# Kernel tuning notes

Measured on AMD Instinct MI355X. Metric: run time of the kernel, lower is better.

The kernel has to match this reference:

```python
import jax, jax.numpy as jnp
import numpy as np
import math

EMBED_DIM = 1024
N1 = 8192
N2 = 8192

def setup_inputs() -> dict:
    key = jax.random.key(0)
    ks = jax.random.split(key, 16)
    D = EMBED_DIM
    s = 1.0 / math.sqrt(D)
    inp = {
        "input_tensor1": jax.random.normal(ks[0], (N1, D), jnp.float32),
        "input_tensor2": jax.random.normal(ks[1], (N2, D), jnp.float32),
    }
    names = ["q1", "k1", "v1", "q2", "k2", "v2"]
    for i, n in enumerate(names):
        inp[f"W{n}"] = jax.random.normal(ks[2 + 2 * i], (D, D), jnp.float32) * s
        inp[f"b{n}"] = jax.random.normal(ks[3 + 2 * i], (D,), jnp.float32) * 0.01
    return inp

def reference(input_tensor1, input_tensor2,
              Wq1, bq1, Wk1, bk1, Wv1, bv1,
              Wq2, bq2, Wk2, bk2, Wv2, bv2):
    D = Wq1.shape[0]
    scale = 1.0 / math.sqrt(D)
    # projections (torch Linear: x @ W^T + b; here W stored pre-transposed)
    q1 = input_tensor1 @ Wq1 + bq1   # [N1, D]
    k1 = input_tensor1 @ Wk1 + bk1   # [N1, D]
    v1 = input_tensor1 @ Wv1 + bv1   # [N1, D]
    q2 = input_tensor2 @ Wq2 + bq2   # [N2, D]
    k2 = input_tensor2 @ Wk2 + bk2   # [N2, D]
    v2 = input_tensor2 @ Wv2 + bv2   # [N2, D]
    # direction 1: tensor2 queries attend to tensor1 keys/values
    probs1 = jax.nn.sigmoid((q2 @ k1.T) * scale)   # [N2, N1]
    ctx1 = probs1 @ v1                              # [N2, D]
    # direction 2: tensor1 queries attend to tensor2 keys/values
    probs2 = jax.nn.sigmoid((q1 @ k2.T) * scale)   # [N1, N2]
    ctx2 = probs2 @ v2                              # [N1, D]
    return (ctx2, probs2, ctx1, probs1)
```

## Files before the change

### kernel.cpp

```cpp
#include <hip/hip_runtime.h>
#include <hip/hip_bf16.h>

#define DIM   1024
#define NTOK  8192

using bf16 = __hip_bfloat16;
typedef __attribute__((ext_vector_type(8))) short bf16x8;
typedef __attribute__((ext_vector_type(4))) float f32x4;

__device__ __forceinline__ unsigned short f2b(float x) {
  union { __hip_bfloat16 h; unsigned short u; } cv;
  cv.h = __float2bfloat16(x);
  return cv.u;
}

__global__ __launch_bounds__(256) void cast_f32_bf16(const float* __restrict__ in,
                                                     bf16* __restrict__ out, int n4) {
  int i = blockIdx.x * 256 + threadIdx.x;
  if (i < n4) {
    const float4 v = ((const float4*)in)[i];
    ushort4 p;
    p.x = f2b(v.x); p.y = f2b(v.y); p.z = f2b(v.z); p.w = f2b(v.w);
    ((ushort4*)out)[i] = p;
  }
}

__global__ __launch_bounds__(256) void transpose_cast32(const float* __restrict__ in,
                                                        bf16* __restrict__ out, int R, int C) {
  __shared__ float t[32][33];
  const int tilesC = C / 32;
  const int c0 = (blockIdx.x % tilesC) * 32;
  const int r0 = (blockIdx.x / tilesC) * 32;
  const int tx = threadIdx.x & 31, ty = threadIdx.x >> 5;
  #pragma unroll
  for (int i = 0; i < 4; ++i) {
    int r = ty + i * 8;
    t[r][tx] = in[(size_t)(r0 + r) * C + c0 + tx];
  }
  __syncthreads();
  #pragma unroll
  for (int i = 0; i < 4; ++i) {
    int cr = ty + i * 8;
    out[(size_t)(c0 + cr) * R + r0 + tx] = __float2bfloat16(t[tx][cr]);
  }
}

__global__ __launch_bounds__(256) void transpose_bf16(const short* __restrict__ in,
                                                      short* __restrict__ out,
                                                      const short* __restrict__ in2,
                                                      short* __restrict__ out2,
                                                      int R, int C) {
  __shared__ short t[64][72];
  const int tilesC = C >> 6;
  const int tilesPer = (R >> 6) * tilesC;
  int bid = blockIdx.x;
  const short* src = in; short* dst = out;
  if (bid >= tilesPer) { bid -= tilesPer; src = in2; dst = out2; }
  const int r0 = (bid / tilesC) << 6, c0 = (bid % tilesC) << 6;
  const int tr = threadIdx.x >> 3, tc8 = (threadIdx.x & 7) << 3;
  #pragma unroll
  for (int p = 0; p < 2; ++p) {
    int r = tr + p * 32;
    int sc = tc8 ^ (((r >> 3) & 7) << 3);
    *(bf16x8*)&t[r][sc] = *(const bf16x8*)&src[(size_t)(r0 + r) * C + c0 + tc8];
  }
  __syncthreads();
  #pragma unroll
  for (int p = 0; p < 2; ++p) {
    int oc = tr + p * 32;
    bf16x8 v;
    #pragma unroll
    for (int e = 0; e < 8; ++e) {
      int a = tc8 + e;
      v[e] = t[a][oc ^ (((a >> 3) & 7) << 3)];
    }
    *(bf16x8*)&dst[(size_t)(c0 + oc) * R + r0 + tc8] = v;
  }
}

__global__ __launch_bounds__(256) void pack_bias(const float* b0, const float* b1,
                                                 const float* b2, const float* b3,
                                                 const float* b4, const float* b5,
                                                 float* __restrict__ out) {
  int i = blockIdx.x * 256 + threadIdx.x;
  if (i < 6 * DIM) {
    int s = i >> 10, o = i & 1023;
    const float* p = (s == 0) ? b0 : (s == 1) ? b1 : (s == 2) ? b2 : (s == 3) ? b3 : (s == 4) ? b4 : b5;
    out[i] = p[o];
  }
}

__global__ __launch_bounds__(256) void add2_dual(const float* __restrict__ p,
                                                 float* __restrict__ o0,
                                                 float* __restrict__ o1, int n4) {
  const size_t MD = (size_t)NTOK * DIM;
  int i = blockIdx.x * 256 + threadIdx.x;
  if (i < 2 * n4) {
    int d = i >= n4;
    int j = i - d * n4;
    const float4 a = ((const float4*)(p + (size_t)d * 2 * MD))[j];
    const float4 b = ((const float4*)(p + (size_t)d * 2 * MD + MD))[j];
    float4 r; r.x = a.x + b.x; r.y = a.y + b.y; r.z = a.z + b.z; r.w = a.w + b.w;
    ((float4*)(d ? o1 : o0))[j] = r;
  }
}

template<int EPI, bool DUAL>
__global__ __launch_bounds__(512, 2) void gemm256(
    const bf16* __restrict__ A,  const bf16* __restrict__ Bt,
    const bf16* __restrict__ A2, const bf16* __restrict__ Bt2,
    int M, int N, int K, int tilesN, int ks, int perDir,
    const float* __restrict__ bias, const float* __restrict__ bias2, float scale,
    float* __restrict__ Cf, float* __restrict__ Cf2,
    bf16* __restrict__ Cb, bf16* __restrict__ Cb2,
    bf16* __restrict__ Cq, bf16* __restrict__ Ck, bf16* __restrict__ Cv,
    bf16* __restrict__ Cq2, bf16* __restrict__ Ck2, bf16* __restrict__ Cv2)
{
  __shared__ bf16 lds[2][2 * 16384];
  const int t    = threadIdx.x;
  const int lane = t & 63, wid = t >> 6;
  const int wr = wid >> 2, wc = wid & 3;
  const int lr = lane & 15, kg = lane >> 4;

  const int nwg = gridDim.x;
  int bid = blockIdx.x;
  { const int q = nwg >> 3; bid = (bid & 7) * q + (bid >> 3); }

  const bf16* Au = A; const bf16* BtU = Bt;
  float* CfU = Cf; bf16* CbU = Cb;
  int bidL = bid;
  if (DUAL && bidL >= perDir) { bidL -= perDir; Au = A2; BtU = Bt2; CfU = Cf2; CbU = Cb2; }
  const int per = perDir / ks;
  const int z   = bidL / per;
  const int rem = bidL % per;
  const int bm  = (rem / tilesN) << 8;
  const int bn  = (rem % tilesN) << 8;
  const int Kc  = K / ks;
  const int NT  = Kc >> 6;
  const size_t kb = (size_t)z * Kc;

  const float* biasU = bias;
  bf16 *CqU = Cq, *CkU = Ck, *CvU = Cv;
  int bmL = bm;
  if (EPI == 5 && bm >= (M >> 1)) {
    BtU = Bt2; biasU = bias2; CqU = Cq2; CkU = Ck2; CvU = Cv2; bmL = bm - (M >> 1);
  }

  const int srow = t >> 3;
  const int scol = ((t & 7) ^ (srow & 7)) * 8;
  const size_t bA = (size_t)(bm + srow) * K + kb + scol;
  const size_t bB = (size_t)(bn + srow) * K + kb + scol;

#define STAGE(buf, isB, R0, tt_) do {                                                   \
    const bf16* g_ = ((isB) ? BtU + bB : Au + bA) + (size_t)(R0) * K + (size_t)(tt_) * 64; \
    __builtin_amdgcn_global_load_lds(                                                   \
        (const __attribute__((address_space(1))) unsigned int*)g_,                      \
        (__attribute__((address_space(3))) unsigned int*)(&lds[buf][((isB) ? 16384 : 0) + (R0) * 64 + t * 8]), \
        16, 0, 0);                                                                      \
  } while (0)

  const int fcol0 = ((kg)     ^ (lr & 7)) * 8;
  const int fcol1 = ((4 + kg) ^ (lr & 7)) * 8;
  const int arow = (wr * 128 + lr) * 64;
  const int brow = (wc * 64 + lr) * 64;

  f32x4 acc[8][4] = {};

  STAGE(0, false, 0, 0);   STAGE(0, false, 128, 0);
  STAGE(0, false, 64, 0);  STAGE(0, false, 192, 0);
  STAGE(0, true, 0, 0);    STAGE(0, true, 64, 0);
  STAGE(0, true, 128, 0);  STAGE(0, true, 192, 0);
  if (NT > 1) {
    STAGE(1, false, 0, 1); STAGE(1, false, 128, 1);
    STAGE(1, true, 0, 1);  STAGE(1, true, 64, 1);
    asm volatile("s_waitcnt vmcnt(4)" ::: "memory");
  } else {
    asm volatile("s_waitcnt vmcnt(0)" ::: "memory");
  }
  __builtin_amdgcn_sched_barrier(0);
  __builtin_amdgcn_s_barrier();

  for (int tt = 0; tt < NT; ++tt) {
    const int cur = tt & 1;
    const bf16* bufA = &lds[cur][0];
    const bf16* bufB = &lds[cur][16384];
    bf16x8 b0[4], b1[4];

    {
      bf16x8 a[4];
      #pragma unroll
      for (int n = 0; n < 4; ++n) b0[n] = *(const bf16x8*)(bufB + brow + n * 1024 + fcol0);
      #pragma unroll
      for (int mi = 0; mi < 4; ++mi) a[mi] = *(const bf16x8*)(bufA + arow + mi * 1024 + fcol0);
      if (tt + 1 < NT) { STAGE(cur ^ 1, true, 128, tt + 1); STAGE(cur ^ 1, true, 192, tt + 1); }
      __builtin_amdgcn_s_barrier();
      asm volatile("s_waitcnt lgkmcnt(0)" ::: "memory");
      __builtin_amdgcn_sched_barrier(0);
      __builtin_amdgcn_s_setprio(1);
      #pragma unroll
      for (int mi = 0; mi < 4; ++mi)
        #pragma unroll
        for (int n = 0; n < 4; ++n)
          acc[mi][n] = __builtin_amdgcn_mfma_f32_16x16x32_bf16(a[mi], b0[n], acc[mi][n], 0, 0, 0);
      __builtin_amdgcn_s_setprio(0);
      __builtin_amdgcn_s_barrier();
    }
    {
      bf16x8 a[4];
      #pragma unroll
      for (int n = 0; n < 4; ++n) b1[n] = *(const bf16x8*)(bufB + brow + n * 1024 + fcol1);
      #pragma unroll
      for (int mi = 0; mi < 4; ++mi) a[mi] = *(const bf16x8*)(bufA + arow + mi * 1024 + fcol1);
      if (tt + 1 < NT) { STAGE(cur ^ 1, false, 64, tt + 1); STAGE(cur ^ 1, false, 192, tt + 1); }
      __builtin_amdgcn_s_barrier();
      asm volatile("s_waitcnt lgkmcnt(0)" ::: "memory");
      __builtin_amdgcn_sched_barrier(0);
      __builtin_amdgcn_s_setprio(1);
      #pragma unroll
      for (int mi = 0; mi < 4; ++mi)
        #pragma unroll
        for (int n = 0; n < 4; ++n)
          acc[mi][n] = __builtin_amdgcn_mfma_f32_16x16x32_bf16(a[mi], b1[n], acc[mi][n], 0, 0, 0);
      __builtin_amdgcn_s_setprio(0);
      __builtin_amdgcn_s_barrier();
    }
    {
      bf16x8 a[4];
      #pragma unroll
      for (int mi = 0; mi < 4; ++mi) a[mi] = *(const bf16x8*)(bufA + arow + 4096 + mi * 1024 + fcol0);
      if (tt + 2 < NT) { STAGE(cur, false, 0, tt + 2); STAGE(cur, false, 128, tt + 2); }
      __builtin_amdgcn_s_barrier();
      asm volatile("s_waitcnt lgkmcnt(0)" ::: "memory");
      __builtin_amdgcn_sched_barrier(0);
      __builtin_amdgcn_s_setprio(1);
      #pragma unroll
      for (int mi = 0; mi < 4; ++mi)
        #pragma unroll
        for (int n = 0; n < 4; ++n)
          acc[4 + mi][n] = __builtin_amdgcn_mfma_f32_16x16x32_bf16(a[mi], b0[n], acc[4 + mi][n], 0, 0, 0);
      __builtin_amdgcn_s_setprio(0);
      __builtin_amdgcn_s_barrier();
    }
    {
      bf16x8 a[4];
      #pragma unroll
      for (int mi = 0; mi < 4; ++mi) a[mi] = *(const bf16x8*)(bufA + arow + 4096 + mi * 1024 + fcol1);
      if (tt + 2 < NT) { STAGE(cur, true, 0, tt + 2); STAGE(cur, true, 64, tt + 2); }
      __builtin_amdgcn_s_barrier();
      asm volatile("s_waitcnt lgkmcnt(0)" ::: "memory");
      __builtin_amdgcn_sched_barrier(0);
      __builtin_amdgcn_s_setprio(1);
      #pragma unroll
      for (int mi = 0; mi < 4; ++mi)
        #pragma unroll
        for (int n = 0; n < 4; ++n)
          acc[4 + mi][n] = __builtin_amdgcn_mfma_f32_16x16x32_bf16(a[mi], b1[n], acc[4 + mi][n], 0, 0, 0);
      __builtin_amdgcn_s_setprio(0);
      if (tt + 2 < NT) { asm volatile("s_waitcnt vmcnt(4)" ::: "memory"); }
      else             { asm volatile("s_waitcnt vmcnt(0)" ::: "memory"); }
      __builtin_amdgcn_sched_barrier(0);
      __builtin_amdgcn_s_barrier();
    }
  }
#undef STAGE

  float* Lf = (float*)&lds[0][0];

  float bN[4];
  if (EPI == 5) {
    #pragma unroll
    for (int n = 0; n < 4; ++n) bN[n] = biasU[bn + wc * 64 + n * 16 + lr];
  }

  #pragma unroll
  for (int h = 0; h < 2; ++h) {
    if (wr == h) {
      #pragma unroll
      for (int m = 0; m < 8; ++m)
        #pragma unroll
        for (int n = 0; n < 4; ++n)
          #pragma unroll
          for (int e = 0; e < 4; ++e) {
            const int lrow = kg * 4 + m * 16 + e;
            const int lcol = wc * 64 + n * 16 + lr;
            float v = acc[m][n][e];
            if (EPI == 2 || EPI == 4) v = 1.0f / (1.0f + __expf(-v * scale));
            if (EPI == 5) v += bN[n];
            Lf[lrow * 256 + (lcol ^ (((lrow >> 2) & 3) << 4))] = v;
          }
    }
    __syncthreads();
    #pragma unroll
    for (int rr = 0; rr < 2; ++rr) {
      const int lrow = wid * 16 + rr * 8 + (lane >> 3);
      (void)lrow;
    }
    #pragma unroll
    for (int rr = 0; rr < 16; ++rr) {
      const int lrow = wid * 16 + rr;
      const int cb   = lane * 4;
      const int cbs  = cb ^ (((lrow >> 2) & 3) << 4);
      const f32x4 v  = *(const f32x4*)&Lf[lrow * 256 + cbs];
      const int gr   = bm + h * 128 + lrow;
      const int gc   = bn + cb;
      if (EPI == 2 || EPI == 4) {
        *(f32x4*)&CfU[(size_t)gr * N + gc] = v;
        if (EPI == 4) {
          ushort4 p; p.x = f2b(v[0]); p.y = f2b(v[1]); p.z = f2b(v[2]); p.w = f2b(v[3]);
          *(ushort4*)&CbU[(size_t)gr * N + gc] = p;
        }
      } else if (EPI == 3) {
        float* Cz = CfU + (size_t)z * ((size_t)M * N);
        *(f32x4*)&Cz[(size_t)gr * N + gc] = v;
      } else if (EPI == 5) {
        const int seg = bn >> 10;
        const int cl  = (bn & 1023) + cb;
        const int r   = bmL + h * 128 + lrow;
        bf16* sel = (seg == 0) ? CqU : (seg == 1) ? CkU : CvU;
        ushort4 p; p.x = f2b(v[0]); p.y = f2b(v[1]); p.z = f2b(v[2]); p.w = f2b(v[3]);
        *(ushort4*)&sel[(size_t)r * DIM + cl] = p;
      }
    }
    __syncthreads();
  }
}

template<int EPI, bool A_F32>
__global__ __launch_bounds__(256) void gemm_nt(
    const void* __restrict__ Ap, const bf16* __restrict__ Bt,
    int M, int N, int K,
    float scale, float* __restrict__ Cf)
{
  __shared__ bf16 As[128 * 32];
  __shared__ bf16 Bs[128 * 32];
  const int tid  = threadIdx.x;
  const int lane = tid & 63, wid = tid >> 6;
  const int wr = wid >> 1, wc = wid & 1;
  const int tilesN = N >> 7;
  const int nwg = gridDim.x;
  int bid = blockIdx.x;
  if ((nwg & 7) == 0) { const int q = nwg >> 3; bid = (bid & 7) * q + (bid >> 3); }
  const int bm = (bid / tilesN) * 128, bn = (bid % tilesN) * 128;
  f32x4 acc[4][4] = {};
  const bf16*  Ab16 = (const bf16*)Ap;
  const float* Af32 = (const float*)Ap;
  const int srow = tid >> 2, sc8 = (tid & 3) * 8;
  const int frow = tid >> 3, fc4 = (tid & 7) * 4;

  for (int k0 = 0; k0 < K; k0 += 32) {
    if (A_F32) {
      #pragma unroll
      for (int is = 0; is < 4; ++is) {
        int row = is * 32 + frow;
        const float4 v = *(const float4*)(Af32 + (size_t)(bm + row) * K + k0 + fc4);
        ushort4 p; p.x = f2b(v.x); p.y = f2b(v.y); p.z = f2b(v.z); p.w = f2b(v.w);
        *(ushort4*)(&As[row * 32 + fc4]) = p;
      }
    } else {
      #pragma unroll
      for (int is = 0; is < 2; ++is) {
        int row = is * 64 + srow;
        const bf16* g = Ab16 + (size_t)(bm + row) * K + k0 + sc8;
        __builtin_amdgcn_global_load_lds(
            (const __attribute__((address_space(1))) unsigned int*)g,
            (__attribute__((address_space(3))) unsigned int*)(&As[row * 32 + sc8]), 16, 0, 0);
      }
    }
    #pragma unroll
    for (int is = 0; is < 2; ++is) {
      int row = is * 64 + srow;
      const bf16* g = Bt + (size_t)(bn + row) * K + k0 + sc8;
      __builtin_amdgcn_global_load_lds(
          (const __attribute__((address_space(1))) unsigned int*)g,
          (__attribute__((address_space(3))) unsigned int*)(&Bs[row * 32 + sc8]), 16, 0, 0);
    }
    __syncthreads();
    const int lr = lane & 15, kg = lane >> 4;
    bf16x8 af[4], bfv[4];
    #pragma unroll
    for (int i = 0; i < 4; ++i)
      af[i] = *(const bf16x8*)(&As[(wr * 64 + i * 16 + lr) * 32 + kg * 8]);
    #pragma unroll
    for (int j = 0; j < 4; ++j)
      bfv[j] = *(const bf16x8*)(&Bs[(wc * 64 + j * 16 + lr) * 32 + kg * 8]);
    #pragma unroll
    for (int i = 0; i < 4; ++i)
      #pragma unroll
      for (int j = 0; j < 4; ++j)
        acc[i][j] = __builtin_amdgcn_mfma_f32_16x16x32_bf16(af[i], bfv[j], acc[i][j], 0, 0, 0);
    __syncthreads();
  }
  const int r0 = bm + wr * 64 + (lane >> 4) * 4;
  const int c0 = bn + wc * 64 + (lane & 15);
  if (EPI == 2) {
    #pragma unroll
    for (int i = 0; i < 4; ++i)
      #pragma unroll
      for (int j = 0; j < 4; ++j)
        #pragma unroll
        for (int e = 0; e < 4; ++e) {
          float pr = 1.0f / (1.0f + __expf(-acc[i][j][e] * scale));
          Cf[(size_t)(r0 + i * 16 + e) * N + c0 + j * 16] = pr;
        }
  } else {
    #pragma unroll
    for (int i = 0; i < 4; ++i)
      #pragma unroll
      for (int j = 0; j < 4; ++j)
        #pragma unroll
        for (int e = 0; e < 4; ++e)
          Cf[(size_t)(r0 + i * 16 + e) * N + c0 + j * 16] = acc[i][j][e];
  }
}

extern "C" void kernel_launch(void* const* d_in, const int* in_sizes, int n_in,
                              void* d_out, int out_size, void* d_ws, size_t ws_size,
                              hipStream_t stream) {
  const float* x1 = (const float*)d_in[0];
  const float* x2 = (const float*)d_in[1];
  const float* W[6] = { (const float*)d_in[2],  (const float*)d_in[4],  (const float*)d_in[6],
                        (const float*)d_in[8],  (const float*)d_in[10], (const float*)d_in[12] };
  const float* B[6] = { (const float*)d_in[3],  (const float*)d_in[5],  (const float*)d_in[7],
                        (const float*)d_in[9],  (const float*)d_in[11], (const float*)d_in[13] };

  const size_t MD = (size_t)NTOK * DIM;
  const size_t DD = (size_t)DIM * DIM;
  const size_t NN = (size_t)NTOK * NTOK;

  bf16* ws   = (bf16*)d_ws;
  bf16* x1b  = ws;
  bf16* x2b  = x1b + MD;
  bf16* wt1  = x2b + MD;
  bf16* wt2  = wt1 + 3 * DD;
  float* bstack = (float*)(wt2 + 3 * DD);
  bf16* q1   = wt2 + 3 * DD + 16384;
  bf16* k1   = q1 + MD;
  bf16* q2   = k1 + MD;
  bf16* k2   = q2 + MD;
  bf16* v1r  = k2 + MD;
  bf16* v2r  = v1r + MD;
  bf16* v1T  = v2r + MD;
  bf16* v2T  = v1T + MD;
  bf16* probsb = v2T + MD;
  float* part  = (float*)(probsb + 2 * NN);

  const size_t topBytes = ((size_t)(12 * MD + 6 * DD + 16384) + 2 * NN) * 2 + 4 * MD * 4;
  const bool top = (ws_size >= topBytes);

  float* out    = (float*)d_out;
  float* ctx2   = out;
  float* probs2 = ctx2 + MD;
  float* ctx1   = probs2 + NN;
  float* probs1 = ctx1 + MD;

  const float scale = 1.0f / 32.0f;

  {
    int n4 = (int)(MD / 4);
    int blks = (n4 + 255) / 256;
    cast_f32_bf16<<<blks, 256, 0, stream>>>(x1, x1b, n4);
    cast_f32_bf16<<<blks, 256, 0, stream>>>(x2, x2b, n4);
  }
  {
    int blks = (DIM / 32) * (DIM / 32);
    transpose_cast32<<<blks, 256, 0, stream>>>(W[0], wt1 + 0 * DD, DIM, DIM);
    transpose_cast32<<<blks, 256, 0, stream>>>(W[1], wt1 + 1 * DD, DIM, DIM);
    transpose_cast32<<<blks, 256, 0, stream>>>(W[2], wt1 + 2 * DD, DIM, DIM);
    transpose_cast32<<<blks, 256, 0, stream>>>(W[3], wt2 + 0 * DD, DIM, DIM);
    transpose_cast32<<<blks, 256, 0, stream>>>(W[4], wt2 + 1 * DD, DIM, DIM);
    transpose_cast32<<<blks, 256, 0, stream>>>(W[5], wt2 + 2 * DD, DIM, DIM);
  }
  pack_bias<<<24, 256, 0, stream>>>(B[0], B[1], B[2], B[3], B[4], B[5], bstack);

  gemm256<5, false><<<64 * 12, 512, 0, stream>>>(
      x1b, wt1, nullptr, wt2, 2 * NTOK, 3 * DIM, DIM, 12, 1, 768,
      bstack, bstack + 3 * DIM, 0.f,
      nullptr, nullptr, nullptr, nullptr,
      q1, k1, v1r, q2, k2, v2r);

  transpose_bf16<<<2 * (NTOK / 64) * (DIM / 64), 256, 0, stream>>>(
      (const short*)v1r, (short*)v1T, (const short*)v2r, (short*)v2T, NTOK, DIM);

  const int perQK = (NTOK / 256) * (NTOK / 256);
  const int perPV = (NTOK / 256) * (DIM / 256);

  if (top) {
    gemm256<4, true><<<2 * perQK, 512, 0, stream>>>(
        q1, k2, q2, k1, NTOK, NTOK, DIM, 32, 1, perQK,
        nullptr, nullptr, scale,
        probs2, probs1, probsb, probsb + NN,
        nullptr, nullptr, nullptr, nullptr, nullptr, nullptr);
    gemm256<3, false><<<2 * perPV, 512, 0, stream>>>(
        probsb, v2T, nullptr, nullptr, NTOK, DIM, NTOK, 4, 2, 2 * perPV,
        nullptr, nullptr, 0.f,
        part, nullptr, nullptr, nullptr,
        nullptr, nullptr, nullptr, nullptr, nullptr, nullptr);
    gemm256<3, false><<<2 * perPV, 512, 0, stream>>>(
        probsb + NN, v1T, nullptr, nullptr, NTOK, DIM, NTOK, 4, 2, 2 * perPV,
        nullptr, nullptr, 0.f,
        part + 2 * MD, nullptr, nullptr, nullptr,
        nullptr, nullptr, nullptr, nullptr, nullptr, nullptr);
    {
      int n4 = (int)(MD / 4);
      add2_dual<<<(2 * n4 + 255) / 256, 256, 0, stream>>>(part, ctx2, ctx1, n4);
    }
  } else {
    gemm256<2, false><<<perQK, 512, 0, stream>>>(
        q1, k2, nullptr, nullptr, NTOK, NTOK, DIM, 32, 1, perQK,
        nullptr, nullptr, scale,
        probs2, nullptr, nullptr, nullptr,
        nullptr, nullptr, nullptr, nullptr, nullptr, nullptr);
    gemm_nt<3, true><<<(NTOK / 128) * (DIM / 128), 256, 0, stream>>>(
        probs2, v2T, NTOK, DIM, NTOK, 0.f, ctx2);
    gemm256<2, false><<<perQK, 512, 0, stream>>>(
        q2, k1, nullptr, nullptr, NTOK, NTOK, DIM, 32, 1, perQK,
        nullptr, nullptr, scale,
        probs1, nullptr, nullptr, nullptr,
        nullptr, nullptr, nullptr, nullptr, nullptr, nullptr);
    gemm_nt<3, true><<<(NTOK / 128) * (DIM / 128), 256, 0, stream>>>(
        probs1, v1T, NTOK, DIM, NTOK, 0.f, ctx1);
  }
}
```

Measured before the change: 831.6 us.

## Replace 256x256 GEMM with 128x128 triple-buffered kernel and drop split-K

Replaces the 512-thread 256x256-tile GEMM with a 256-thread 128x128-tile kernel that keeps three LDS stages over 32-wide K steps. It uses grouped tile ordering and nontemporal stores for the large fp32 outputs. The PV GEMMs for both directions now run as one dual launch without split-K, which removes the partial buffers and the add2_dual reduction kernel. Smaller tiles give more occupancy and less tail waste, but each tile reuses its operands less and the kernel issues more global loads.

```diff
diff --git a/kernel.cpp b/kernel.cpp
--- a/kernel.cpp
+++ b/kernel.cpp
@@ -90,36 +90,25 @@
   }
 }
 
-__global__ __launch_bounds__(256) void add2_dual(const float* __restrict__ p,
-                                                 float* __restrict__ o0,
-                                                 float* __restrict__ o1, int n4) {
-  const size_t MD = (size_t)NTOK * DIM;
-  int i = blockIdx.x * 256 + threadIdx.x;
-  if (i < 2 * n4) {
-    int d = i >= n4;
-    int j = i - d * n4;
-    const float4 a = ((const float4*)(p + (size_t)d * 2 * MD))[j];
-    const float4 b = ((const float4*)(p + (size_t)d * 2 * MD + MD))[j];
-    float4 r; r.x = a.x + b.x; r.y = a.y + b.y; r.z = a.z + b.z; r.w = a.w + b.w;
-    ((float4*)(d ? o1 : o0))[j] = r;
-  }
-}
-
 template<int EPI, bool DUAL>
-__global__ __launch_bounds__(512, 2) void gemm256(
+__global__ __launch_bounds__(256, 3) void gemm128(
     const bf16* __restrict__ A,  const bf16* __restrict__ Bt,
     const bf16* __restrict__ A2, const bf16* __restrict__ Bt2,
-    int M, int N, int K, int tilesN, int ks, int perDir,
+    int M, int N, int K, int TM, int perDir,
     const float* __restrict__ bias, const float* __restrict__ bias2, float scale,
     float* __restrict__ Cf, float* __restrict__ Cf2,
     bf16* __restrict__ Cb, bf16* __restrict__ Cb2,
     bf16* __restrict__ Cq, bf16* __restrict__ Ck, bf16* __restrict__ Cv,
     bf16* __restrict__ Cq2, bf16* __restrict__ Ck2, bf16* __restrict__ Cv2)
 {
-  __shared__ bf16 lds[2][2 * 16384];
+  __shared__ __align__(16) char smem[49152];
+  bf16* sA = (bf16*)smem;
+  bf16* sB = (bf16*)(smem + 24576);
+  float* Lf = (float*)smem;
+
   const int t    = threadIdx.x;
   const int lane = t & 63, wid = t >> 6;
-  const int wr = wid >> 2, wc = wid & 3;
+  const int wr = wid >> 1, wc = wid & 1;
   const int lr = lane & 15, kg = lane >> 4;
 
   const int nwg = gridDim.x;
@@ -128,16 +117,12 @@
 
   const bf16* Au = A; const bf16* BtU = Bt;
   float* CfU = Cf; bf16* CbU = Cb;
-  int bidL = bid;
-  if (DUAL && bidL >= perDir) { bidL -= perDir; Au = A2; BtU = Bt2; CfU = Cf2; CbU = Cb2; }
-  const int per = perDir / ks;
-  const int z   = bidL / per;
-  const int rem = bidL % per;
-  const int bm  = (rem / tilesN) << 8;
-  const int bn  = (rem % tilesN) << 8;
-  const int Kc  = K / ks;
-  const int NT  = Kc >> 6;
-  const size_t kb = (size_t)z * Kc;
+  if (DUAL && bid >= perDir) { bid -= perDir; Au = A2; BtU = Bt2; CfU = Cf2; CbU = Cb2; }
+
+  const int gw = TM << 3;
+  const int s  = bid / gw, w = bid % gw;
+  const int bm = (w >> 3) << 7;
+  const int bn = ((s << 3) + (w & 7)) << 7;
 
   const float* biasU = bias;
   bf16 *CqU = Cq, *CkU = Ck, *CvU = Cv;
@@ -146,176 +131,103 @@
     BtU = Bt2; biasU = bias2; CqU = Cq2; CkU = Ck2; CvU = Cv2; bmL = bm - (M >> 1);
   }
 
-  const int srow = t >> 3;
-  const int scol = ((t & 7) ^ (srow & 7)) * 8;
-  const size_t bA = (size_t)(bm + srow) * K + kb + scol;
-  const size_t bB = (size_t)(bn + srow) * K + kb + scol;
-
-#define STAGE(buf, isB, R0, tt_) do {                                                   \
-    const bf16* g_ = ((isB) ? BtU + bB : Au + bA) + (size_t)(R0) * K + (size_t)(tt_) * 64; \
-    __builtin_amdgcn_global_load_lds(                                                   \
-        (const __attribute__((address_space(1))) unsigned int*)g_,                      \
-        (__attribute__((address_space(3))) unsigned int*)(&lds[buf][((isB) ? 16384 : 0) + (R0) * 64 + t * 8]), \
-        16, 0, 0);                                                                      \
-  } while (0)
-
-  const int fcol0 = ((kg)     ^ (lr & 7)) * 8;
-  const int fcol1 = ((4 + kg) ^ (lr & 7)) * 8;
-  const int arow = (wr * 128 + lr) * 64;
-  const int brow = (wc * 64 + lr) * 64;
-
-  f32x4 acc[8][4] = {};
-
-  STAGE(0, false, 0, 0);   STAGE(0, false, 128, 0);
-  STAGE(0, false, 64, 0);  STAGE(0, false, 192, 0);
-  STAGE(0, true, 0, 0);    STAGE(0, true, 64, 0);
-  STAGE(0, true, 128, 0);  STAGE(0, true, 192, 0);
-  if (NT > 1) {
-    STAGE(1, false, 0, 1); STAGE(1, false, 128, 1);
-    STAGE(1, true, 0, 1);  STAGE(1, true, 64, 1);
-    asm volatile("s_waitcnt vmcnt(4)" ::: "memory");
-  } else {
-    asm volatile("s_waitcnt vmcnt(0)" ::: "memory");
-  }
+  const int srow = t >> 2;
+  const int scol = (t & 3) * 8;
+  const size_t gA = (size_t)(bm + srow) * K + scol;
+  const size_t gB = (size_t)(bn + srow) * K + scol;
+
+#define STAGE(slot, isB, R0, tt_) \
+  __builtin_amdgcn_global_load_lds( \
+    (const __attribute__((address_space(1))) unsigned int*)(((isB) ? BtU + gB : Au + gA) + (size_t)(R0) * K + (size_t)(tt_) * 32), \
+    (__attribute__((address_space(3))) unsigned int*)(((isB) ? sB : sA) + (slot) * 4096 + (R0) * 32 + t * 8), \
+    16, 0, 0)
+
+  const int aoff = (wr * 64 + lr) * 32 + kg * 8;
+  const int boff = (wc * 64 + lr) * 32 + kg * 8;
+
+  f32x4 acc[4][4] = {};
+  const int NT = K >> 5;
+
+  STAGE(0, 0, 0, 0); STAGE(0, 0, 64, 0); STAGE(0, 1, 0, 0); STAGE(0, 1, 64, 0);
+  STAGE(1, 0, 0, 1); STAGE(1, 0, 64, 1); STAGE(1, 1, 0, 1); STAGE(1, 1, 64, 1);
+  asm volatile("s_waitcnt vmcnt(4)" ::: "memory");
   __builtin_amdgcn_sched_barrier(0);
   __builtin_amdgcn_s_barrier();
 
+  int cur = 0, stg = 2;
   for (int tt = 0; tt < NT; ++tt) {
-    const int cur = tt & 1;
-    const bf16* bufA = &lds[cur][0];
-    const bf16* bufB = &lds[cur][16384];
-    bf16x8 b0[4], b1[4];
-
-    {
-      bf16x8 a[4];
-      #pragma unroll
-      for (int n = 0; n < 4; ++n) b0[n] = *(const bf16x8*)(bufB + brow + n * 1024 + fcol0);
-      #pragma unroll
-      for (int mi = 0; mi < 4; ++mi) a[mi] = *(const bf16x8*)(bufA + arow + mi * 1024 + fcol0);
-      if (tt + 1 < NT) { STAGE(cur ^ 1, true, 128, tt + 1); STAGE(cur ^ 1, true, 192, tt + 1); }
-      __builtin_amdgcn_s_barrier();
-      asm volatile("s_waitcnt lgkmcnt(0)" ::: "memory");
-      __builtin_amdgcn_sched_barrier(0);
-      __builtin_amdgcn_s_setprio(1);
-      #pragma unroll
-      for (int mi = 0; mi < 4; ++mi)
-        #pragma unroll
-        for (int n = 0; n < 4; ++n)
-          acc[mi][n] = __builtin_amdgcn_mfma_f32_16x16x32_bf16(a[mi], b0[n], acc[mi][n], 0, 0, 0);
-      __builtin_amdgcn_s_setprio(0);
-      __builtin_amdgcn_s_barrier();
-    }
-    {
-      bf16x8 a[4];
-      #pragma unroll
-      for (int n = 0; n < 4; ++n) b1[n] = *(const bf16x8*)(bufB + brow + n * 1024 + fcol1);
-      #pragma unroll
-      for (int mi = 0; mi < 4; ++mi) a[mi] = *(const bf16x8*)(bufA + arow + mi * 1024 + fcol1);
-      if (tt + 1 < NT) { STAGE(cur ^ 1, false, 64, tt + 1); STAGE(cur ^ 1, false, 192, tt + 1); }
-      __builtin_amdgcn_s_barrier();
-      asm volatile("s_waitcnt lgkmcnt(0)" ::: "memory");
-      __builtin_amdgcn_sched_barrier(0);
-      __builtin_amdgcn_s_setprio(1);
-      #pragma unroll
-      for (int mi = 0; mi < 4; ++mi)
-        #pragma unroll
-        for (int n = 0; n < 4; ++n)
-          acc[mi][n] = __builtin_amdgcn_mfma_f32_16x16x32_bf16(a[mi], b1[n], acc[mi][n], 0, 0, 0);
-      __builtin_amdgcn_s_setprio(0);
-      __builtin_amdgcn_s_barrier();
-    }
-    {
-      bf16x8 a[4];
-      #pragma unroll
-      for (int mi = 0; mi < 4; ++mi) a[mi] = *(const bf16x8*)(bufA + arow + 4096 + mi * 1024 + fcol0);
-      if (tt + 2 < NT) { STAGE(cur, false, 0, tt + 2); STAGE(cur, false, 128, tt + 2); }
-      __builtin_amdgcn_s_barrier();
-      asm volatile("s_waitcnt lgkmcnt(0)" ::: "memory");
-      __builtin_amdgcn_sched_barrier(0);
-      __builtin_amdgcn_s_setprio(1);
-      #pragma unroll
-      for (int mi = 0; mi < 4; ++mi)
-        #pragma unroll
-        for (int n = 0; n < 4; ++n)
-          acc[4 + mi][n] = __builtin_amdgcn_mfma_f32_16x16x32_bf16(a[mi], b0[n], acc[4 + mi][n], 0, 0, 0);
-      __builtin_amdgcn_s_setprio(0);
-      __builtin_amdgcn_s_barrier();
-    }
-    {
-      bf16x8 a[4];
-      #pragma unroll
-      for (int mi = 0; mi < 4; ++mi) a[mi] = *(const bf16x8*)(bufA + arow + 4096 + mi * 1024 + fcol1);
-      if (tt + 2 < NT) { STAGE(cur, true, 0, tt + 2); STAGE(cur, true, 64, tt + 2); }
-      __builtin_amdgcn_s_barrier();
-      asm volatile("s_waitcnt lgkmcnt(0)" ::: "memory");
-      __builtin_amdgcn_sched_barrier(0);
-      __builtin_amdgcn_s_setprio(1);
-      #pragma unroll
-      for (int mi = 0; mi < 4; ++mi)
-        #pragma unroll
-        for (int n = 0; n < 4; ++n)
-          acc[4 + mi][n] = __builtin_amdgcn_mfma_f32_16x16x32_bf16(a[mi], b1[n], acc[4 + mi][n], 0, 0, 0);
-      __builtin_amdgcn_s_setprio(0);
-      if (tt + 2 < NT) { asm volatile("s_waitcnt vmcnt(4)" ::: "memory"); }
-      else             { asm volatile("s_waitcnt vmcnt(0)" ::: "memory"); }
-      __builtin_amdgcn_sched_barrier(0);
-      __builtin_amdgcn_s_barrier();
-    }
+    bf16x8 a[4], b[4];
+    const bf16* pa = sA + cur * 4096 + aoff;
+    const bf16* pb = sB + cur * 4096 + boff;
+    #pragma unroll
+    for (int i = 0; i < 4; ++i) a[i] = *(const bf16x8*)(pa + i * 512);
+    #pragma unroll
+    for (int i = 0; i < 4; ++i) b[i] = *(const bf16x8*)(pb + i * 512);
+    if (tt + 2 < NT) {
+      STAGE(stg, 0, 0, tt + 2); STAGE(stg, 0, 64, tt + 2);
+      STAGE(stg, 1, 0, tt + 2); STAGE(stg, 1, 64, tt + 2);
+    }
+    __builtin_amdgcn_s_barrier();
+    asm volatile("s_waitcnt lgkmcnt(0)" ::: "memory");
+    __builtin_amdgcn_sched_barrier(0);
+    __builtin_amdgcn_s_setprio(1);
+    #pragma unroll
+    for (int mi = 0; mi < 4; ++mi)
+      #pragma unroll
+      for (int n = 0; n < 4; ++n)
+        acc[mi][n] = __builtin_amdgcn_mfma_f32_16x16x32_bf16(a[mi], b[n], acc[mi][n], 0, 0, 0);
+    __builtin_amdgcn_s_setprio(0);
+    if (tt + 2 < NT) { asm volatile("s_waitcnt vmcnt(4)" ::: "memory"); }
+    else             { asm volatile("s_waitcnt vmcnt(0)" ::: "memory"); }
+    __builtin_amdgcn_sched_barrier(0);
+    __builtin_amdgcn_s_barrier();
+    cur = (cur == 2) ? 0 : cur + 1;
+    stg = (stg == 2) ? 0 : stg + 1;
   }
 #undef STAGE
 
-  float* Lf = (float*)&lds[0][0];
-
-  float bN[4];
+  float bv[4];
   if (EPI == 5) {
     #pragma unroll
-    for (int n = 0; n < 4; ++n) bN[n] = biasU[bn + wc * 64 + n * 16 + lr];
+    for (int n = 0; n < 4; ++n) bv[n] = biasU[bn + wc * 64 + n * 16 + lr];
   }
 
   #pragma unroll
   for (int h = 0; h < 2; ++h) {
     if (wr == h) {
       #pragma unroll
-      for (int m = 0; m < 8; ++m)
+      for (int mi = 0; mi < 4; ++mi)
         #pragma unroll
         for (int n = 0; n < 4; ++n)
           #pragma unroll
           for (int e = 0; e < 4; ++e) {
-            const int lrow = kg * 4 + m * 16 + e;
+            const int lrow = mi * 16 + kg * 4 + e;
             const int lcol = wc * 64 + n * 16 + lr;
-            float v = acc[m][n][e];
+            float v = acc[mi][n][e];
             if (EPI == 2 || EPI == 4) v = 1.0f / (1.0f + __expf(-v * scale));
-            if (EPI == 5) v += bN[n];
-            Lf[lrow * 256 + (lcol ^ (((lrow >> 2) & 3) << 4))] = v;
+            if (EPI == 5) v += bv[n];
+            Lf[lrow * 128 + lcol] = v;
           }
     }
     __syncthreads();
     #pragma unroll
-    for (int rr = 0; rr < 2; ++rr) {
-      const int lrow = wid * 16 + rr * 8 + (lane >> 3);
-      (void)lrow;
-    }
-    #pragma unroll
-    for (int rr = 0; rr < 16; ++rr) {
-      const int lrow = wid * 16 + rr;
-      const int cb   = lane * 4;
-      const int cbs  = cb ^ (((lrow >> 2) & 3) << 4);
-      const f32x4 v  = *(const f32x4*)&Lf[lrow * 256 + cbs];
-      const int gr   = bm + h * 128 + lrow;
-      const int gc   = bn + cb;
+    for (int rr = 0; rr < 8; ++rr) {
+      const int lrow = wid * 16 + rr * 2 + (lane >> 5);
+      const int col  = (lane & 31) * 4;
+      const f32x4 v = *(const f32x4*)&Lf[lrow * 128 + col];
+      const int gr = bm + h * 64 + lrow;
       if (EPI == 2 || EPI == 4) {
-        *(f32x4*)&CfU[(size_t)gr * N + gc] = v;
+        __builtin_nontemporal_store(v, (f32x4*)&CfU[(size_t)gr * N + bn + col]);
         if (EPI == 4) {
           ushort4 p; p.x = f2b(v[0]); p.y = f2b(v[1]); p.z = f2b(v[2]); p.w = f2b(v[3]);
-          *(ushort4*)&CbU[(size_t)gr * N + gc] = p;
+          *(ushort4*)&CbU[(size_t)gr * N + bn + col] = p;
         }
       } else if (EPI == 3) {
-        float* Cz = CfU + (size_t)z * ((size_t)M * N);
-        *(f32x4*)&Cz[(size_t)gr * N + gc] = v;
+        __builtin_nontemporal_store(v, (f32x4*)&CfU[(size_t)gr * N + bn + col]);
       } else if (EPI == 5) {
         const int seg = bn >> 10;
-        const int cl  = (bn & 1023) + cb;
-        const int r   = bmL + h * 128 + lrow;
+        const int cl  = (bn & 1023) + col;
+        const int r   = bmL + h * 64 + lrow;
         bf16* sel = (seg == 0) ? CqU : (seg == 1) ? CkU : CvU;
         ushort4 p; p.x = f2b(v[0]); p.y = f2b(v[1]); p.z = f2b(v[2]); p.w = f2b(v[3]);
         *(ushort4*)&sel[(size_t)r * DIM + cl] = p;
@@ -335,7 +247,7 @@
   __shared__ bf16 Bs[128 * 32];
   const int tid  = threadIdx.x;
   const int lane = tid & 63, wid = tid >> 6;
-  const int wr = wid >> 1, wc = wid & 1;
+  const int wrr = wid >> 1, wcc = wid & 1;
   const int tilesN = N >> 7;
   const int nwg = gridDim.x;
   int bid = blockIdx.x;
@@ -375,14 +287,14 @@
           (__attribute__((address_space(3))) unsigned int*)(&Bs[row * 32 + sc8]), 16, 0, 0);
     }
     __syncthreads();
-    const int lr = lane & 15, kg = lane >> 4;
+    const int lrr = lane & 15, kgg = lane >> 4;
     bf16x8 af[4], bfv[4];
     #pragma unroll
     for (int i = 0; i < 4; ++i)
-      af[i] = *(const bf16x8*)(&As[(wr * 64 + i * 16 + lr) * 32 + kg * 8]);
+      af[i] = *(const bf16x8*)(&As[(wrr * 64 + i * 16 + lrr) * 32 + kgg * 8]);
     #pragma unroll
     for (int j = 0; j < 4; ++j)
-      bfv[j] = *(const bf16x8*)(&Bs[(wc * 64 + j * 16 + lr) * 32 + kg * 8]);
+      bfv[j] = *(const bf16x8*)(&Bs[(wcc * 64 + j * 16 + lrr) * 32 + kgg * 8]);
     #pragma unroll
     for (int i = 0; i < 4; ++i)
       #pragma unroll
@@ -390,8 +302,8 @@
         acc[i][j] = __builtin_amdgcn_mfma_f32_16x16x32_bf16(af[i], bfv[j], acc[i][j], 0, 0, 0);
     __syncthreads();
   }
-  const int r0 = bm + wr * 64 + (lane >> 4) * 4;
-  const int c0 = bn + wc * 64 + (lane & 15);
+  const int r0 = bm + wrr * 64 + (lane >> 4) * 4;
+  const int c0 = bn + wcc * 64 + (lane & 15);
   if (EPI == 2) {
     #pragma unroll
     for (int i = 0; i < 4; ++i)
@@ -442,9 +354,8 @@
   bf16* v1T  = v2r + MD;
   bf16* v2T  = v1T + MD;
   bf16* probsb = v2T + MD;
-  float* part  = (float*)(probsb + 2 * NN);
-
-  const size_t topBytes = ((size_t)(12 * MD + 6 * DD + 16384) + 2 * NN) * 2 + 4 * MD * 4;
+
+  const size_t topBytes = ((size_t)(10 * MD + 6 * DD + 16384) + 2 * NN) * 2;
   const bool top = (ws_size >= topBytes);
 
   float* out    = (float*)d_out;
@@ -472,8 +383,8 @@
   }
   pack_bias<<<24, 256, 0, stream>>>(B[0], B[1], B[2], B[3], B[4], B[5], bstack);
 
-  gemm256<5, false><<<64 * 12, 512, 0, stream>>>(
-      x1b, wt1, nullptr, wt2, 2 * NTOK, 3 * DIM, DIM, 12, 1, 768,
+  gemm128<5, false><<<128 * 24, 256, 0, stream>>>(
+      x1b, wt1, nullptr, wt2, 2 * NTOK, 3 * DIM, DIM, 128, 3072,
       bstack, bstack + 3 * DIM, 0.f,
       nullptr, nullptr, nullptr, nullptr,
       q1, k1, v1r, q2, k2, v2r);
@@ -481,39 +392,30 @@
   transpose_bf16<<<2 * (NTOK / 64) * (DIM / 64), 256, 0, stream>>>(
       (const short*)v1r, (short*)v1T, (const short*)v2r, (short*)v2T, NTOK, DIM);
 
-  const int perQK = (NTOK / 256) * (NTOK / 256);
-  const int perPV = (NTOK / 256) * (DIM / 256);
+  const int perQK = (NTOK / 128) * (NTOK / 128);
+  const int perPV = (NTOK / 128) * (DIM / 128);
 
   if (top) {
-    gemm256<4, true><<<2 * perQK, 512, 0, stream>>>(
-        q1, k2, q2, k1, NTOK, NTOK, DIM, 32, 1, perQK,
+    gemm128<4, true><<<2 * perQK, 256, 0, stream>>>(
+        q1, k2, q2, k1, NTOK, NTOK, DIM, 64, perQK,
         nullptr, nullptr, scale,
         probs2, probs1, probsb, probsb + NN,
         nullptr, nullptr, nullptr, nullptr, nullptr, nullptr);
-    gemm256<3, false><<<2 * perPV, 512, 0, stream>>>(
-        probsb, v2T, nullptr, nullptr, NTOK, DIM, NTOK, 4, 2, 2 * perPV,
+    gemm128<3, true><<<2 * perPV, 256, 0, stream>>>(
+        probsb, v2T, probsb + NN, v1T, NTOK, DIM, NTOK, 64, perPV,
         nullptr, nullptr, 0.f,
-        part, nullptr, nullptr, nullptr,
+        ctx2, ctx1, nullptr, nullptr,
         nullptr, nullptr, nullptr, nullptr, nullptr, nullptr);
-    gemm256<3, false><<<2 * perPV, 512, 0, stream>>>(
-        probsb + NN, v1T, nullptr, nullptr, NTOK, DIM, NTOK, 4, 2, 2 * perPV,
-        nullptr, nullptr, 0.f,
-        part + 2 * MD, nullptr, nullptr, nullptr,
-        nullptr, nullptr, nullptr, nullptr, nullptr, nullptr);
-    {
-      int n4 = (int)(MD / 4);
-      add2_dual<<<(2 * n4 + 255) / 256, 256, 0, stream>>>(part, ctx2, ctx1, n4);
-    }
   } else {
-    gemm256<2, false><<<perQK, 512, 0, stream>>>(
-        q1, k2, nullptr, nullptr, NTOK, NTOK, DIM, 32, 1, perQK,
+    gemm128<2, false><<<perQK, 256, 0, stream>>>(
+        q1, k2, nullptr, nullptr, NTOK, NTOK, DIM, 64, perQK,
         nullptr, nullptr, scale,
         probs2, nullptr, nullptr, nullptr,
         nullptr, nullptr, nullptr, nullptr, nullptr, nullptr);
     gemm_nt<3, true><<<(NTOK / 128) * (DIM / 128), 256, 0, stream>>>(
         probs2, v2T, NTOK, DIM, NTOK, 0.f, ctx2);
-    gemm256<2, false><<<perQK, 512, 0, stream>>>(
-        q2, k1, nullptr, nullptr, NTOK, NTOK, DIM, 32, 1, perQK,
+    gemm128<2, false><<<perQK, 256, 0, stream>>>(
+        q2, k1, nullptr, nullptr, NTOK, NTOK, DIM, 64, perQK,
         nullptr, nullptr, scale,
         probs1, nullptr, nullptr, nullptr,
         nullptr, nullptr, nullptr, nullptr, nullptr, nullptr);
```

Result: slower. 888.8 us (+6.9%).

## Drop split-K in PV GEMM, merge both directions into one launch

Applied to the files above, without the earlier changes.

The PV GEMMs previously split K in two, wrote fp32 partials and summed them in a separate add kernel. Now one dual-direction launch computes the full K per tile and writes ctx directly, removing the partial buffer traffic and the extra kernel. It also switches fp32 output stores to nontemporal and relaxes launch bounds to one workgroup per SIMD pair. The trade-off is only 128 workgroups for the PV stage, which may underfill the GPU, and the launch-bounds change may affect occupancy in every gemm256 instance.

```diff
diff --git a/kernel.cpp b/kernel.cpp
--- a/kernel.cpp
+++ b/kernel.cpp
@@ -90,26 +90,11 @@
   }
 }
 
-__global__ __launch_bounds__(256) void add2_dual(const float* __restrict__ p,
-                                                 float* __restrict__ o0,
-                                                 float* __restrict__ o1, int n4) {
-  const size_t MD = (size_t)NTOK * DIM;
-  int i = blockIdx.x * 256 + threadIdx.x;
-  if (i < 2 * n4) {
-    int d = i >= n4;
-    int j = i - d * n4;
-    const float4 a = ((const float4*)(p + (size_t)d * 2 * MD))[j];
-    const float4 b = ((const float4*)(p + (size_t)d * 2 * MD + MD))[j];
-    float4 r; r.x = a.x + b.x; r.y = a.y + b.y; r.z = a.z + b.z; r.w = a.w + b.w;
-    ((float4*)(d ? o1 : o0))[j] = r;
-  }
-}
-
 template<int EPI, bool DUAL>
-__global__ __launch_bounds__(512, 2) void gemm256(
+__global__ __launch_bounds__(512, 1) void gemm256(
     const bf16* __restrict__ A,  const bf16* __restrict__ Bt,
     const bf16* __restrict__ A2, const bf16* __restrict__ Bt2,
-    int M, int N, int K, int tilesN, int ks, int perDir,
+    int M, int N, int K, int tilesN, int perDir,
     const float* __restrict__ bias, const float* __restrict__ bias2, float scale,
     float* __restrict__ Cf, float* __restrict__ Cf2,
     bf16* __restrict__ Cb, bf16* __restrict__ Cb2,
@@ -128,16 +113,10 @@
 
   const bf16* Au = A; const bf16* BtU = Bt;
   float* CfU = Cf; bf16* CbU = Cb;
-  int bidL = bid;
-  if (DUAL && bidL >= perDir) { bidL -= perDir; Au = A2; BtU = Bt2; CfU = Cf2; CbU = Cb2; }
-  const int per = perDir / ks;
-  const int z   = bidL / per;
-  const int rem = bidL % per;
-  const int bm  = (rem / tilesN) << 8;
-  const int bn  = (rem % tilesN) << 8;
-  const int Kc  = K / ks;
-  const int NT  = Kc >> 6;
-  const size_t kb = (size_t)z * Kc;
+  if (DUAL && bid >= perDir) { bid -= perDir; Au = A2; BtU = Bt2; CfU = Cf2; CbU = Cb2; }
+
+  const int bm = (bid / tilesN) << 8;
+  const int bn = (bid % tilesN) << 8;
 
   const float* biasU = bias;
   bf16 *CqU = Cq, *CkU = Ck, *CvU = Cv;
@@ -148,8 +127,8 @@
 
   const int srow = t >> 3;
   const int scol = ((t & 7) ^ (srow & 7)) * 8;
-  const size_t bA = (size_t)(bm + srow) * K + kb + scol;
-  const size_t bB = (size_t)(bn + srow) * K + kb + scol;
+  const size_t bA = (size_t)(bm + srow) * K + scol;
+  const size_t bB = (size_t)(bn + srow) * K + scol;
 
 #define STAGE(buf, isB, R0, tt_) do {                                                   \
     const bf16* g_ = ((isB) ? BtU + bB : Au + bA) + (size_t)(R0) * K + (size_t)(tt_) * 64; \
@@ -165,6 +144,7 @@
   const int brow = (wc * 64 + lr) * 64;
 
   f32x4 acc[8][4] = {};
+  const int NT = K >> 6;
 
   STAGE(0, false, 0, 0);   STAGE(0, false, 128, 0);
   STAGE(0, false, 64, 0);  STAGE(0, false, 192, 0);
@@ -291,11 +271,6 @@
     }
     __syncthreads();
     #pragma unroll
-    for (int rr = 0; rr < 2; ++rr) {
-      const int lrow = wid * 16 + rr * 8 + (lane >> 3);
-      (void)lrow;
-    }
-    #pragma unroll
     for (int rr = 0; rr < 16; ++rr) {
       const int lrow = wid * 16 + rr;
       const int cb   = lane * 4;
@@ -304,14 +279,13 @@
       const int gr   = bm + h * 128 + lrow;
       const int gc   = bn + cb;
       if (EPI == 2 || EPI == 4) {
-        *(f32x4*)&CfU[(size_t)gr * N + gc] = v;
+        __builtin_nontemporal_store(v, (f32x4*)&CfU[(size_t)gr * N + gc]);
         if (EPI == 4) {
           ushort4 p; p.x = f2b(v[0]); p.y = f2b(v[1]); p.z = f2b(v[2]); p.w = f2b(v[3]);
           *(ushort4*)&CbU[(size_t)gr * N + gc] = p;
         }
       } else if (EPI == 3) {
-        float* Cz = CfU + (size_t)z * ((size_t)M * N);
-        *(f32x4*)&Cz[(size_t)gr * N + gc] = v;
+        __builtin_nontemporal_store(v, (f32x4*)&CfU[(size_t)gr * N + gc]);
       } else if (EPI == 5) {
         const int seg = bn >> 10;
         const int cl  = (bn & 1023) + cb;
@@ -335,7 +309,7 @@
   __shared__ bf16 Bs[128 * 32];
   const int tid  = threadIdx.x;
   const int lane = tid & 63, wid = tid >> 6;
-  const int wr = wid >> 1, wc = wid & 1;
+  const int wrr = wid >> 1, wcc = wid & 1;
   const int tilesN = N >> 7;
   const int nwg = gridDim.x;
   int bid = blockIdx.x;
@@ -375,14 +349,14 @@
           (__attribute__((address_space(3))) unsigned int*)(&Bs[row * 32 + sc8]), 16, 0, 0);
     }
     __syncthreads();
-    const int lr = lane & 15, kg = lane >> 4;
+    const int lrr = lane & 15, kgg = lane >> 4;
     bf16x8 af[4], bfv[4];
     #pragma unroll
     for (int i = 0; i < 4; ++i)
-      af[i] = *(const bf16x8*)(&As[(wr * 64 + i * 16 + lr) * 32 + kg * 8]);
+      af[i] = *(const bf16x8*)(&As[(wrr * 64 + i * 16 + lrr) * 32 + kgg * 8]);
     #pragma unroll
     for (int j = 0; j < 4; ++j)
-      bfv[j] = *(const bf16x8*)(&Bs[(wc * 64 + j * 16 + lr) * 32 + kg * 8]);
+      bfv[j] = *(const bf16x8*)(&Bs[(wcc * 64 + j * 16 + lrr) * 32 + kgg * 8]);
     #pragma unroll
     for (int i = 0; i < 4; ++i)
       #pragma unroll
@@ -390,8 +364,8 @@
         acc[i][j] = __builtin_amdgcn_mfma_f32_16x16x32_bf16(af[i], bfv[j], acc[i][j], 0, 0, 0);
     __syncthreads();
   }
-  const int r0 = bm + wr * 64 + (lane >> 4) * 4;
-  const int c0 = bn + wc * 64 + (lane & 15);
+  const int r0 = bm + wrr * 64 + (lane >> 4) * 4;
+  const int c0 = bn + wcc * 64 + (lane & 15);
   if (EPI == 2) {
     #pragma unroll
     for (int i = 0; i < 4; ++i)
@@ -442,9 +416,8 @@
   bf16* v1T  = v2r + MD;
   bf16* v2T  = v1T + MD;
   bf16* probsb = v2T + MD;
-  float* part  = (float*)(probsb + 2 * NN);
-
-  const size_t topBytes = ((size_t)(12 * MD + 6 * DD + 16384) + 2 * NN) * 2 + 4 * MD * 4;
+
+  const size_t topBytes = ((size_t)(10 * MD + 6 * DD + 16384) + 2 * NN) * 2;
   const bool top = (ws_size >= topBytes);
 
   float* out    = (float*)d_out;
@@ -473,7 +446,7 @@
   pack_bias<<<24, 256, 0, stream>>>(B[0], B[1], B[2], B[3], B[4], B[5], bstack);
 
   gemm256<5, false><<<64 * 12, 512, 0, stream>>>(
-      x1b, wt1, nullptr, wt2, 2 * NTOK, 3 * DIM, DIM, 12, 1, 768,
+      x1b, wt1, nullptr, wt2, 2 * NTOK, 3 * DIM, DIM, 12, 768,
       bstack, bstack + 3 * DIM, 0.f,
       nullptr, nullptr, nullptr, nullptr,
       q1, k1, v1r, q2, k2, v2r);
@@ -486,34 +459,25 @@
 
   if (top) {
     gemm256<4, true><<<2 * perQK, 512, 0, stream>>>(
-        q1, k2, q2, k1, NTOK, NTOK, DIM, 32, 1, perQK,
+        q1, k2, q2, k1, NTOK, NTOK, DIM, 32, perQK,
         nullptr, nullptr, scale,
         probs2, probs1, probsb, probsb + NN,
         nullptr, nullptr, nullptr, nullptr, nullptr, nullptr);
-    gemm256<3, false><<<2 * perPV, 512, 0, stream>>>(
-        probsb, v2T, nullptr, nullptr, NTOK, DIM, NTOK, 4, 2, 2 * perPV,
+    gemm256<3, true><<<2 * perPV, 512, 0, stream>>>(
+        probsb, v2T, probsb + NN, v1T, NTOK, DIM, NTOK, 4, perPV,
         nullptr, nullptr, 0.f,
-        part, nullptr, nullptr, nullptr,
+        ctx2, ctx1, nullptr, nullptr,
         nullptr, nullptr, nullptr, nullptr, nullptr, nullptr);
-    gemm256<3, false><<<2 * perPV, 512, 0, stream>>>(
-        probsb + NN, v1T, nullptr, nullptr, NTOK, DIM, NTOK, 4, 2, 2 * perPV,
-        nullptr, nullptr, 0.f,
-        part + 2 * MD, nullptr, nullptr, nullptr,
-        nullptr, nullptr, nullptr, nullptr, nullptr, nullptr);
-    {
-      int n4 = (int)(MD / 4);
-      add2_dual<<<(2 * n4 + 255) / 256, 256, 0, stream>>>(part, ctx2, ctx1, n4);
-    }
   } else {
     gemm256<2, false><<<perQK, 512, 0, stream>>>(
-        q1, k2, nullptr, nullptr, NTOK, NTOK, DIM, 32, 1, perQK,
+        q1, k2, nullptr, nullptr, NTOK, NTOK, DIM, 32, perQK,
         nullptr, nullptr, scale,
         probs2, nullptr, nullptr, nullptr,
         nullptr, nullptr, nullptr, nullptr, nullptr, nullptr);
     gemm_nt<3, true><<<(NTOK / 128) * (DIM / 128), 256, 0, stream>>>(
         probs2, v2T, NTOK, DIM, NTOK, 0.f, ctx2);
     gemm256<2, false><<<perQK, 512, 0, stream>>>(
-        q2, k1, nullptr, nullptr, NTOK, NTOK, DIM, 32, 1, perQK,
+        q2, k1, nullptr, nullptr, NTOK, NTOK, DIM, 32, perQK,
         nullptr, nullptr, scale,
         probs1, nullptr, nullptr, nullptr,
         nullptr, nullptr, nullptr, nullptr, nullptr, nullptr);
```

Measured after the change: 772.4 us. 7.1% less time.
